# Optimization experiments

Measured on AMD Instinct MI355X. Metric: run time of the kernel, lower is better.

Reference implementation:

```python
import jax, jax.numpy as jnp
import numpy as np

B, S, D = 2, 1024, 1024
L, E, F = 2, 8, 2048


def setup_inputs() -> dict:
    key = jax.random.key(0)
    kx, kp, k1, k2 = jax.random.split(key, 4)
    x = jax.random.normal(kx, (B, S, D), dtype=jnp.float32)
    # prototypes scaled so dot products are O(1), keeping softmax well-behaved
    protos = jax.random.normal(kp, (L, E, D), dtype=jnp.float32) / np.sqrt(D)
    W1 = jax.random.normal(k1, (L, E, D, F), dtype=jnp.float32) * 0.02
    W2 = jax.random.normal(k2, (L, E, F, D), dtype=jnp.float32) * 0.02
    return {"x": x, "protos": protos, "W1": W1, "W2": W2, "k": 2}


def _route(x, protos_l, k):
    # expert_mapping: abs(dot(prototype, input)) per expert, keep top-k, rest -> -inf, softmax
    scores = jnp.abs(jnp.einsum("bsd,ed->bse", x, protos_l))  # [B,S,E]
    topv, _ = jax.lax.top_k(scores, k)
    thresh = topv[..., -1:]  # k-th largest per token
    masked = jnp.where(scores >= thresh, scores, -jnp.inf)
    return jax.nn.softmax(masked, axis=-1)  # [B,S,E]


def reference(x, protos, W1, W2, k):
    n_layers = protos.shape[0]
    for l in range(n_layers):  # fixed small layer loop
        w = _route(x, protos[l], k)  # [B,S,E]
        h = jax.nn.relu(jnp.einsum("bsd,edf->bsef", x, W1[l]))  # [B,S,E,F]
        y = jnp.einsum("bsef,efd,bse->bsd", h, W2[l], w)  # weighted expert mix
        x = x + y
    return x
```

## Files before the change

kernel.cpp:

```cpp
#include <hip/hip_runtime.h>
#include <hip/hip_bf16.h>
#include <cstdint>

#define T_TOKENS 2048
#define DDIM 1024
#define FDIM 2048
#define NEXP 8
#define BMPAD 64
#define RMAX 4608
#define RALLOC 4736

#define ATILE_EL 2048
#define BTILE_EL 4096

typedef unsigned short u16;
typedef short bf16x8 __attribute__((ext_vector_type(8)));
typedef u16 u16x8 __attribute__((ext_vector_type(8)));
typedef u16 u16x4v __attribute__((ext_vector_type(4)));
typedef float f32x4 __attribute__((ext_vector_type(4)));

#define VMCNT(n) asm volatile("s_waitcnt vmcnt(" #n ")" ::: "memory")
#define SB() __builtin_amdgcn_sched_barrier(0)
#define BAR() __builtin_amdgcn_s_barrier()

__device__ __forceinline__ u16 bf16_rn(float f) {
  unsigned u = __builtin_bit_cast(unsigned, f);
  u += 0x7fffu + ((u >> 16) & 1u);
  return (u16)(u >> 16);
}
__device__ __forceinline__ float bf16_f(u16 h) {
  unsigned u = ((unsigned)h) << 16;
  return __builtin_bit_cast(float, u);
}
__device__ __forceinline__ void gl16(const void* g, void* l) {
  __builtin_amdgcn_global_load_lds((const __attribute__((address_space(1))) void*)g,
                                   (__attribute__((address_space(3))) void*)l, 16, 0, 0);
}

template <int GX, int GY, int GZ>
__device__ __forceinline__ void swz3(unsigned lin, int& bx, int& by, int& bz) {
  constexpr unsigned nwg = (unsigned)GX * GY * GZ;
  const unsigned nl = (lin & 7u) * (nwg >> 3) + (lin >> 3);
  bx = nl % GX;
  const unsigned t = nl / GX;
  by = t % GY;
  bz = t / GY;
}


template <bool LO>
__device__ __forceinline__ void wconv_dev(
    int nb, int kb, int e, const float* __restrict__ W, u16* __restrict__ Hi,
    u16* __restrict__ Lo, int K, int N, float* tile ) {
  const float* Wp = W + ((size_t)e * K + (size_t)kb * 32) * N + nb * 128;
  const int t = threadIdx.x;
#pragma unroll
  for (int i = 0; i < 4; ++i) {
    const int f4 = i * 256 + t;
    const int kr = f4 >> 5;
    const int c4 = (f4 & 31) * 4;
    float4 v = *(const float4*)(Wp + (size_t)kr * N + c4);
    *(float4*)&tile[kr * 129 + c4] = v;
  }
  __syncthreads();
  const size_t tb = (((size_t)e * (N >> 7) + nb) * (K >> 5) + kb) * BTILE_EL;
#pragma unroll
  for (int j = 0; j < 2; ++j) {
    const int cid = j * 256 + t;
    const int n = cid & 127, ksel = cid >> 7;
    u16x8 hv, lv;
#pragma unroll
    for (int i = 0; i < 8; ++i) {
      float f = tile[(ksel * 8 + i) * 129 + n];
      u16 h = bf16_rn(f);
      hv[i] = h;
      if (LO) lv[i] = bf16_rn(f - bf16_f(h));
    }
    *(u16x8*)(Hi + tb + (size_t)cid * 8) = hv;
    if (LO) *(u16x8*)(Lo + tb + (size_t)cid * 8) = lv;
  }
}

__device__ __forceinline__ void wconv_p_dev(
    int nb, int kb, int e, const float* __restrict__ W, u16* __restrict__ Hi,
    const float* __restrict__ proto2, float* __restrict__ Ppart, int K, int N,
    float* smem) {
  float* tile = smem;
  float* pr = smem + 32 * 129;
  const float* Wp = W + ((size_t)e * K + (size_t)kb * 32) * N + nb * 128;
  const int t = threadIdx.x;
#pragma unroll
  for (int i = 0; i < 4; ++i) {
    const int f4 = i * 256 + t;
    const int kr = f4 >> 5;
    const int c4 = (f4 & 31) * 4;
    float4 v = *(const float4*)(Wp + (size_t)kr * N + c4);
    *(float4*)&tile[kr * 129 + c4] = v;
  }
  {
    const int idx = t * 4;
    const int e2 = idx >> 7, n = idx & 127;
    *(float4*)&pr[e2 * 128 + n] =
        *(const float4*)(proto2 + (size_t)e2 * DDIM + nb * 128 + n);
  }
  __syncthreads();
  const size_t tb = (((size_t)e * (N >> 7) + nb) * (K >> 5) + kb) * BTILE_EL;
#pragma unroll
  for (int j = 0; j < 2; ++j) {
    const int cid = j * 256 + t;
    const int n = cid & 127, ksel = cid >> 7;
    u16x8 hv;
#pragma unroll
    for (int i = 0; i < 8; ++i) hv[i] = bf16_rn(tile[(ksel * 8 + i) * 129 + n]);
    *(u16x8*)(Hi + tb + (size_t)cid * 8) = hv;
  }
  const int e2 = t >> 5, f = t & 31;
  float s = 0.f;
#pragma unroll 16
  for (int n = 0; n < 128; ++n) s += tile[f * 129 + n] * pr[e2 * 128 + n];
  Ppart[(((size_t)nb * NEXP + e) * NEXP + e2) * FDIM + kb * 32 + f] = s;
}

template <bool LO>
__device__ __forceinline__ void gather_dev(
    int r, const float* __restrict__ x, const int* __restrict__ row2token,
    u16* __restrict__ Ahi, u16* __restrict__ Alo) {
  const int t = row2token[r];
  const int c = threadIdx.x * 4;
  float4 v = make_float4(0.f, 0.f, 0.f, 0.f);
  if (t >= 0) v = *(const float4*)(x + (size_t)t * DDIM + c);
  float vv[4] = {v.x, v.y, v.z, v.w};
  u16x4v hi, lo;
#pragma unroll
  for (int i = 0; i < 4; ++i) {
    u16 h = bf16_rn(vv[i]);
    hi[i] = h;
    if (LO) lo[i] = bf16_rn(vv[i] - bf16_f(h));
  }
  const size_t el = ((size_t)(r >> 6) * (DDIM >> 5) + (c >> 5)) * ATILE_EL +
                    (size_t)(((c >> 3) & 3) * 64 + (r & 63)) * 8 + (c & 7);
  *(u16x4v*)(Ahi + el) = hi;
  if (LO) *(u16x4v*)(Alo + el) = lo;
}

__device__ __forceinline__ void gemm_split_dev(
    unsigned lin, u16* lds, const u16* __restrict__ Ahi, const u16* __restrict__ Alo,
    const u16* __restrict__ Bhi, const u16* __restrict__ Blo,
    u16* __restrict__ OutHi, u16* __restrict__ OutLo,
    const int* __restrict__ cnt, const int* __restrict__ offp, int K, int N) {
  int bx, by, bz;
  swz3<FDIM / 128, RMAX / 64, NEXP>(lin, bx, by, bz);
  const int e = bz;
  const int cp = (cnt[e] + 63) & ~63;
  if (by * 64 >= cp) return;
  const int row0 = offp[e] + by * 64;
  const int n0 = bx * 128;
  const int nkb = K >> 5;
  constexpr int BUF_EL = 12288;

  const int tid = threadIdx.x;
  const int lane = tid & 63;
  const int wid = tid >> 6;
  const int wr = wid >> 1, wc = wid & 1;
  const int lr = lane & 15, kg = lane >> 4;
  const int lo16 = lane << 4;

  f32x4 acc[2][4];
#pragma unroll
  for (int i = 0; i < 2; ++i)
#pragma unroll
    for (int j = 0; j < 4; ++j)
#pragma unroll
      for (int r = 0; r < 4; ++r) acc[i][j][r] = 0.f;

  const size_t abase = (size_t)(row0 >> 6) * nkb;
  const size_t bbase = ((size_t)e * (N >> 7) + (n0 >> 7)) * nkb;

  auto STAGE = [&](int kb, int b) {
    char* d = (char*)(lds + b * BUF_EL);
    const char* gah = (const char*)(Ahi + (abase + kb) * ATILE_EL);
    const char* gal = (const char*)(Alo + (abase + kb) * ATILE_EL);
    const char* gbh = (const char*)(Bhi + (bbase + kb) * BTILE_EL);
    const char* gbl = (const char*)(Blo + (bbase + kb) * BTILE_EL);
    if (wid == 0) {
      gl16(gah + 0 * 1024 + lo16, d + 0 * 1024);
      gl16(gah + 1 * 1024 + lo16, d + 1 * 1024);
      gl16(gah + 2 * 1024 + lo16, d + 2 * 1024);
      gl16(gah + 3 * 1024 + lo16, d + 3 * 1024);
      gl16(gal + 0 * 1024 + lo16, d + 4096 + 0 * 1024);
      gl16(gal + 1 * 1024 + lo16, d + 4096 + 1 * 1024);
    } else if (wid == 1) {
      gl16(gal + 2 * 1024 + lo16, d + 4096 + 2 * 1024);
      gl16(gal + 3 * 1024 + lo16, d + 4096 + 3 * 1024);
      gl16(gbh + 0 * 1024 + lo16, d + 8192 + 0 * 1024);
      gl16(gbh + 1 * 1024 + lo16, d + 8192 + 1 * 1024);
      gl16(gbh + 2 * 1024 + lo16, d + 8192 + 2 * 1024);
      gl16(gbh + 3 * 1024 + lo16, d + 8192 + 3 * 1024);
    } else if (wid == 2) {
      gl16(gbh + 4 * 1024 + lo16, d + 8192 + 4 * 1024);
      gl16(gbh + 5 * 1024 + lo16, d + 8192 + 5 * 1024);
      gl16(gbh + 6 * 1024 + lo16, d + 8192 + 6 * 1024);
      gl16(gbh + 7 * 1024 + lo16, d + 8192 + 7 * 1024);
      gl16(gbl + 0 * 1024 + lo16, d + 16384 + 0 * 1024);
      gl16(gbl + 1 * 1024 + lo16, d + 16384 + 1 * 1024);
    } else {
      gl16(gbl + 2 * 1024 + lo16, d + 16384 + 2 * 1024);
      gl16(gbl + 3 * 1024 + lo16, d + 16384 + 3 * 1024);
      gl16(gbl + 4 * 1024 + lo16, d + 16384 + 4 * 1024);
      gl16(gbl + 5 * 1024 + lo16, d + 16384 + 5 * 1024);
      gl16(gbl + 6 * 1024 + lo16, d + 16384 + 6 * 1024);
      gl16(gbl + 7 * 1024 + lo16, d + 16384 + 7 * 1024);
    }
  };

  STAGE(0, 0);
  int cur = 0;
  for (int kb = 0; kb < nkb; ++kb) {
    const bool pf = (kb + 1 < nkb);
    if (pf) STAGE(kb + 1, cur ^ 1);
    if (pf) { VMCNT(6); } else { VMCNT(0); }
    SB(); BAR(); SB();

    const u16* buf = lds + cur * BUF_EL;
    const u16* AsH = buf;
    const u16* AsL = buf + 2048;
    const u16* BsH = buf + 4096;
    const u16* BsL = buf + 8192;
    const int arow = (kg * 64 + wr * 32 + lr) * 8;
    const int bcol = (kg * 128 + wc * 64 + lr) * 8;

    bf16x8 ah0 = *(const bf16x8*)&AsH[arow];
    bf16x8 ah1 = *(const bf16x8*)&AsH[arow + 128];
    bf16x8 bh[4];
#pragma unroll
    for (int j = 0; j < 4; ++j) bh[j] = *(const bf16x8*)&BsH[bcol + j * 128];
#pragma unroll
    for (int j = 0; j < 4; ++j) {
      acc[0][j] = __builtin_amdgcn_mfma_f32_16x16x32_bf16(ah0, bh[j], acc[0][j], 0, 0, 0);
      acc[1][j] = __builtin_amdgcn_mfma_f32_16x16x32_bf16(ah1, bh[j], acc[1][j], 0, 0, 0);
    }
    bf16x8 al0 = *(const bf16x8*)&AsL[arow];
    bf16x8 al1 = *(const bf16x8*)&AsL[arow + 128];
#pragma unroll
    for (int j = 0; j < 4; ++j) {
      bf16x8 bl = *(const bf16x8*)&BsL[bcol + j * 128];
      acc[0][j] = __builtin_amdgcn_mfma_f32_16x16x32_bf16(ah0, bl, acc[0][j], 0, 0, 0);
      acc[1][j] = __builtin_amdgcn_mfma_f32_16x16x32_bf16(ah1, bl, acc[1][j], 0, 0, 0);
      acc[0][j] = __builtin_amdgcn_mfma_f32_16x16x32_bf16(al0, bh[j], acc[0][j], 0, 0, 0);
      acc[1][j] = __builtin_amdgcn_mfma_f32_16x16x32_bf16(al1, bh[j], acc[1][j], 0, 0, 0);
    }
    SB(); BAR(); SB();
    cur ^= 1;
  }

  const int nkbO = N >> 5;
#pragma unroll
  for (int i = 0; i < 2; ++i) {
#pragma unroll
    for (int j = 0; j < 4; ++j) {
      const int Cj = n0 + wc * 64 + j * 16 + lr;
      f32x4 v = acc[i][j];
#pragma unroll
      for (int r = 0; r < 4; ++r) {
        const int R = row0 + wr * 32 + i * 16 + kg * 4 + r;
        float f = fmaxf(v[r], 0.f);
        const size_t el = ((size_t)(R >> 6) * nkbO + (Cj >> 5)) * ATILE_EL +
                          (size_t)(((Cj >> 3) & 3) * 64 + (R & 63)) * 8 + (Cj & 7);
        u16 h = bf16_rn(f);
        OutHi[el] = h;
        OutLo[el] = bf16_rn(f - bf16_f(h));
      }
    }
  }
}

template <int GX, int GY, bool RELU, int OUTMODE>
__device__ __forceinline__ void gemm_plain_dev(
    unsigned lin, u16* lds, const u16* __restrict__ Ahi, const u16* __restrict__ Bhi,
    u16* __restrict__ OutHi, float* __restrict__ OutF,
    const int* __restrict__ cnt, const int* __restrict__ offp, int K, int N) {
  int bx, by, bz;
  swz3<GX, GY, NEXP>(lin, bx, by, bz);
  const int e = bz;
  const int cp = (cnt[e] + 63) & ~63;
  if (by * 128 >= cp) return;
  const int row0 = offp[e] + by * 128;
  const int rend = offp[e] + cp;
  const int n0 = bx * 128;
  const int nkb = K >> 5;
  constexpr int BUF_EL = 8192;

  const int tid = threadIdx.x;
  const int lane = tid & 63;
  const int wid = tid >> 6;
  const int wr = wid >> 1, wc = wid & 1;
  const int lr = lane & 15, kg = lane >> 4;
  const int lo16 = lane << 4;

  f32x4 acc[4][4];
#pragma unroll
  for (int i = 0; i < 4; ++i)
#pragma unroll
    for (int j = 0; j < 4; ++j)
#pragma unroll
      for (int r = 0; r < 4; ++r) acc[i][j][r] = 0.f;

  const int at0 = row0 >> 6;
  const size_t bbase = ((size_t)e * (N >> 7) + (n0 >> 7)) * nkb;

  auto STAGE = [&](int kb, int b) {
    char* d = (char*)(lds + b * BUF_EL);
    if (wid < 2) {
      const char* g = (const char*)(Ahi + ((size_t)(at0 + wid) * nkb + kb) * ATILE_EL);
      gl16(g + 0 * 1024 + lo16, d + wid * 4096 + 0 * 1024);
      gl16(g + 1 * 1024 + lo16, d + wid * 4096 + 1 * 1024);
      gl16(g + 2 * 1024 + lo16, d + wid * 4096 + 2 * 1024);
      gl16(g + 3 * 1024 + lo16, d + wid * 4096 + 3 * 1024);
    } else {
      const char* g = (const char*)(Bhi + (bbase + kb) * BTILE_EL) + (wid - 2) * 4096;
      gl16(g + 0 * 1024 + lo16, d + 8192 + (wid - 2) * 4096 + 0 * 1024);
      gl16(g + 1 * 1024 + lo16, d + 8192 + (wid - 2) * 4096 + 1 * 1024);
      gl16(g + 2 * 1024 + lo16, d + 8192 + (wid - 2) * 4096 + 2 * 1024);
      gl16(g + 3 * 1024 + lo16, d + 8192 + (wid - 2) * 4096 + 3 * 1024);
    }
  };

  STAGE(0, 0);
  int cur = 0;
  for (int kb = 0; kb < nkb; ++kb) {
    const bool pf = (kb + 1 < nkb);
    if (pf) STAGE(kb + 1, cur ^ 1);
    if (pf) { VMCNT(4); } else { VMCNT(0); }
    SB(); BAR(); SB();

    const u16* buf = lds + cur * BUF_EL;
    const u16* AsH = buf + wr * 2048;
    const u16* BsH = buf + 4096;
    const int arow = (kg * 64 + lr) * 8;
    const int bcol = (kg * 128 + wc * 64 + lr) * 8;

    bf16x8 ah[4], bh[4];
#pragma unroll
    for (int i = 0; i < 4; ++i) ah[i] = *(const bf16x8*)&AsH[arow + i * 128];
#pragma unroll
    for (int j = 0; j < 4; ++j) bh[j] = *(const bf16x8*)&BsH[bcol + j * 128];
#pragma unroll
    for (int i = 0; i < 4; ++i)
#pragma unroll
      for (int j = 0; j < 4; ++j)
        acc[i][j] = __builtin_amdgcn_mfma_f32_16x16x32_bf16(ah[i], bh[j], acc[i][j], 0, 0, 0);
    SB(); BAR(); SB();
    cur ^= 1;
  }

  const int nkbO = N >> 5;
#pragma unroll
  for (int i = 0; i < 4; ++i) {
#pragma unroll
    for (int j = 0; j < 4; ++j) {
      const int Cj = n0 + wc * 64 + j * 16 + lr;
      f32x4 v = acc[i][j];
#pragma unroll
      for (int r = 0; r < 4; ++r) {
        const int R = row0 + wr * 64 + i * 16 + kg * 4 + r;
        if (R >= rend) continue;
        float f = v[r];
        if (RELU) f = fmaxf(f, 0.f);
        if constexpr (OUTMODE == 0) {
          OutF[(size_t)R * N + Cj] = f;
        } else {
          const size_t el = ((size_t)(R >> 6) * nkbO + (Cj >> 5)) * ATILE_EL +
                            (size_t)(((Cj >> 3) & 3) * 64 + (R & 63)) * 8 + (Cj & 7);
          OutHi[el] = bf16_rn(f);
        }
      }
    }
  }
}


__global__ __launch_bounds__(256) void route_kernel(
    const float* __restrict__ x, const float* __restrict__ protos,
    int* __restrict__ eid, float* __restrict__ wgt) {
  const int t = blockIdx.x;
  const int tid = threadIdx.x;
  __shared__ float red[NEXP][256];
  const float4 xv = ((const float4*)(x + (size_t)t * DDIM))[tid];
  float acc[NEXP];
#pragma unroll
  for (int e = 0; e < NEXP; ++e) {
    const float4 p = ((const float4*)protos)[e * 256 + tid];
    acc[e] = xv.x * p.x + xv.y * p.y + xv.z * p.z + xv.w * p.w;
  }
#pragma unroll
  for (int e = 0; e < NEXP; ++e) red[e][tid] = acc[e];
  __syncthreads();
  for (int s = 128; s > 0; s >>= 1) {
    if (tid < s) {
#pragma unroll
      for (int e = 0; e < NEXP; ++e) red[e][tid] += red[e][tid + s];
    }
    __syncthreads();
  }
  if (tid == 0) {
    float m1 = -1.f, m2 = -1.f;
    int i1 = 0, i2 = 0;
#pragma unroll
    for (int e = 0; e < NEXP; ++e) {
      float s = fabsf(red[e][0]);
      if (s > m1) { m2 = m1; i2 = i1; m1 = s; i1 = e; }
      else if (s > m2) { m2 = s; i2 = e; }
    }
    float e2 = __expf(m2 - m1);
    float z = 1.f + e2;
    eid[t * 2] = i1;
    eid[t * 2 + 1] = i2;
    wgt[t * 2] = 1.f / z;
    wgt[t * 2 + 1] = e2 / z;
  }
}

__global__ __launch_bounds__(256) void route2_kernel(
    const float* __restrict__ x, const float* __restrict__ protos2,
    const u16* __restrict__ h_hi, const u16* __restrict__ h_lo,
    const float* __restrict__ P, const int* __restrict__ eidA,
    const int* __restrict__ pos, const float* __restrict__ wgtA,
    int* __restrict__ eidB, float* __restrict__ wgtB) {
  const int t = blockIdx.x;
  const int tid = threadIdx.x;
  __shared__ float red[NEXP][256];
  const float4 xv = ((const float4*)(x + (size_t)t * DDIM))[tid];
  float acc[NEXP];
#pragma unroll
  for (int e = 0; e < NEXP; ++e) {
    const float4 p = ((const float4*)protos2)[e * 256 + tid];
    acc[e] = xv.x * p.x + xv.y * p.y + xv.z * p.z + xv.w * p.w;
  }
  const int p0 = pos[t * 2], p1 = pos[t * 2 + 1];
  const int e0 = eidA[t * 2], e1 = eidA[t * 2 + 1];
  const float w0 = wgtA[t * 2], w1 = wgtA[t * 2 + 1];
  const int f0 = tid * 8;
  const int nkbF = FDIM >> 5;
  float h0[8], h1[8];
  {
    const size_t el0 = ((size_t)(p0 >> 6) * nkbF + (f0 >> 5)) * ATILE_EL +
                       (size_t)((((f0 >> 3) & 3) * 64 + (p0 & 63)) * 8);
    const size_t el1 = ((size_t)(p1 >> 6) * nkbF + (f0 >> 5)) * ATILE_EL +
                       (size_t)((((f0 >> 3) & 3) * 64 + (p1 & 63)) * 8);
    u16x8 a = *(const u16x8*)&h_hi[el0], b = *(const u16x8*)&h_lo[el0];
    u16x8 c = *(const u16x8*)&h_hi[el1], d = *(const u16x8*)&h_lo[el1];
#pragma unroll
    for (int j = 0; j < 8; ++j) {
      h0[j] = bf16_f(a[j]) + bf16_f(b[j]);
      h1[j] = bf16_f(c[j]) + bf16_f(d[j]);
    }
  }
#pragma unroll
  for (int e2 = 0; e2 < NEXP; ++e2) {
    const float* P0 = P + ((size_t)(e0 * NEXP + e2)) * FDIM + f0;
    const float* P1 = P + ((size_t)(e1 * NEXP + e2)) * FDIM + f0;
    float c = 0.f;
#pragma unroll
    for (int j = 0; j < 8; ++j) c += w0 * h0[j] * P0[j] + w1 * h1[j] * P1[j];
    acc[e2] += c;
  }
#pragma unroll
  for (int e = 0; e < NEXP; ++e) red[e][tid] = acc[e];
  __syncthreads();
  for (int s = 128; s > 0; s >>= 1) {
    if (tid < s) {
#pragma unroll
      for (int e = 0; e < NEXP; ++e) red[e][tid] += red[e][tid + s];
    }
    __syncthreads();
  }
  if (tid == 0) {
    float m1 = -1.f, m2 = -1.f;
    int i1 = 0, i2 = 0;
#pragma unroll
    for (int e = 0; e < NEXP; ++e) {
      float s = fabsf(red[e][0]);
      if (s > m1) { m2 = m1; i2 = i1; m1 = s; i1 = e; }
      else if (s > m2) { m2 = s; i2 = e; }
    }
    float e2 = __expf(m2 - m1);
    float z = 1.f + e2;
    eidB[t * 2] = i1;
    eidB[t * 2 + 1] = i2;
    wgtB[t * 2] = 1.f / z;
    wgtB[t * 2 + 1] = e2 / z;
  }
}

__device__ __forceinline__ void compact_dev(
    const int* __restrict__ eid, int* __restrict__ cnt, int* __restrict__ offp,
    int* __restrict__ row2token, int* __restrict__ pos, int* lcnt ) {
  int* s_off = lcnt + NEXP * 256;
  int* s_tot = s_off + NEXP;
  const int tid = threadIdx.x;
  const int base = tid * 16;
  int my[16];
#pragma unroll
  for (int i = 0; i < 4; ++i)
    *(int4*)&my[i * 4] = *(const int4*)(eid + base + i * 4);
#pragma unroll
  for (int e = 0; e < NEXP; ++e) {
    int c = 0;
#pragma unroll
    for (int i = 0; i < 16; ++i) c += (my[i] == e) ? 1 : 0;
    lcnt[e * 256 + tid] = c;
  }
  for (int r = tid; r < RMAX; r += 256) row2token[r] = -1;
  __syncthreads();
  if (tid < NEXP) {
    int run = 0;
    for (int i = 0; i < 256; ++i) {
      int v = lcnt[tid * 256 + i];
      lcnt[tid * 256 + i] = run;
      run += v;
    }
    s_tot[tid] = run;
  }
  __syncthreads();
  if (tid == 0) {
    int o = 0;
    for (int e = 0; e < NEXP; ++e) {
      s_off[e] = o;
      o += (s_tot[e] + BMPAD - 1) & ~(BMPAD - 1);
    }
  }
  __syncthreads();
  int myoff[NEXP];
#pragma unroll
  for (int e = 0; e < NEXP; ++e) myoff[e] = s_off[e] + lcnt[e * 256 + tid];
#pragma unroll
  for (int i = 0; i < 16; ++i) {
    int r = 0;
#pragma unroll
    for (int e = 0; e < NEXP; ++e) r = (my[i] == e) ? myoff[e] : r;
    row2token[r] = (base + i) >> 1;
    pos[base + i] = r;
#pragma unroll
    for (int e = 0; e < NEXP; ++e) myoff[e] += (my[i] == e) ? 1 : 0;
  }
  if (tid < NEXP) {
    cnt[tid] = s_tot[tid];
    offp[tid] = s_off[tid];
  }
}

__global__ __launch_bounds__(256) void compact_kernel(
    const int* __restrict__ eid, int* __restrict__ cnt, int* __restrict__ offp,
    int* __restrict__ row2token, int* __restrict__ pos) {
  __shared__ int lcnt[NEXP * 256 + 16];
  compact_dev(eid, cnt, offp, row2token, pos, lcnt);
}

__global__ __launch_bounds__(256) void fusedC1_kernel(
    const float* __restrict__ W1, u16* __restrict__ W_hi, u16* __restrict__ W_lo,
    const float* __restrict__ x, const int* __restrict__ row2token,
    u16* __restrict__ Ag_hi, u16* __restrict__ Ag_lo) {
  __shared__ float smem[32 * 129];
  const unsigned lin = blockIdx.x;
  if (lin < 4096u) {
    const int nb = lin % 16;
    const int kb = (lin / 16) % 32;
    const int e = lin / 512;
    wconv_dev<true>(nb, kb, e, W1, W_hi, W_lo, DDIM, FDIM, smem);
  } else {
    gather_dev<true>((int)(lin - 4096u), x, row2token, Ag_hi, Ag_lo);
  }
}

__global__ __launch_bounds__(256, 3) void fusedC2_kernel(
    const u16* __restrict__ Ag_hi, const u16* __restrict__ Ag_lo,
    const u16* __restrict__ W_hi, const u16* __restrict__ W_lo,
    u16* __restrict__ h_hi, u16* __restrict__ h_lo,
    const int* __restrict__ cnt, const int* __restrict__ offp,
    const float* __restrict__ W2, u16* __restrict__ W2A,
    const float* __restrict__ proto2, float* __restrict__ Ppart) {
  __shared__ u16 lds[2 * 12288];
  const unsigned lin = blockIdx.x;
  if (lin < 9216u) {
    gemm_split_dev(lin, lds, Ag_hi, Ag_lo, W_hi, W_lo, h_hi, h_lo, cnt, offp,
                   DDIM, FDIM);
  } else {
    const unsigned l2 = lin - 9216u;
    const int nb = l2 % 8;
    const int kb = (l2 / 8) % 64;
    const int e = l2 / 512;
    wconv_p_dev(nb, kb, e, W2, W2A, proto2, Ppart, FDIM, DDIM, (float*)lds);
  }
}

__global__ __launch_bounds__(256, 4) void fusedC3_kernel(
    const u16* __restrict__ h_hi, const u16* __restrict__ W2A,
    float* __restrict__ part, const int* __restrict__ cnt, const int* __restrict__ offp,
    const float* __restrict__ W1b, u16* __restrict__ W_lo,
    const float* __restrict__ W2b, u16* __restrict__ W_hi,
    const float* __restrict__ Ppart, float* __restrict__ P) {
  __shared__ u16 lds[2 * 8192];
  const unsigned lin = blockIdx.x;
  if (lin < 2304u) {
    gemm_plain_dev<DDIM / 128, RMAX / 128, false, 0>(
        lin, lds, h_hi, W2A, nullptr, part, cnt, offp, FDIM, DDIM);
  } else if (lin < 6400u) {
    const unsigned l2 = lin - 2304u;
    wconv_dev<false>(l2 % 16, (l2 / 16) % 32, l2 / 512, W1b, W_lo, nullptr,
                     DDIM, FDIM, (float*)lds);
  } else if (lin < 10496u) {
    const unsigned l2 = lin - 6400u;
    wconv_dev<false>(l2 % 8, (l2 / 8) % 64, l2 / 512, W2b, W_hi, nullptr,
                     FDIM, DDIM, (float*)lds);
  } else {
    const int i = (int)(lin - 10496u) * 256 + threadIdx.x;
    float s = 0.f;
#pragma unroll
    for (int nb = 0; nb < 8; ++nb) s += Ppart[(size_t)nb * (NEXP * NEXP * FDIM) + i];
    P[i] = s;
  }
}

__global__ __launch_bounds__(256) void fusedD_kernel(
    const float* __restrict__ part, const int* __restrict__ pos,
    const float* __restrict__ wgt, float* __restrict__ x,
    const int* __restrict__ eidB, int* __restrict__ cnt, int* __restrict__ offp,
    int* __restrict__ row2token, int* __restrict__ posB) {
  __shared__ int lcnt[NEXP * 256 + 16];
  const unsigned lin = blockIdx.x;
  if (lin < 2048u) {
    const int t = lin;
    const int c = threadIdx.x * 4;
    const int p0 = pos[t * 2], p1 = pos[t * 2 + 1];
    const float w0 = wgt[t * 2], w1 = wgt[t * 2 + 1];
    float4 xa = *(float4*)(x + (size_t)t * DDIM + c);
    const float4 y0 = *(const float4*)(part + (size_t)p0 * DDIM + c);
    const float4 y1 = *(const float4*)(part + (size_t)p1 * DDIM + c);
    xa.x += w0 * y0.x + w1 * y1.x;
    xa.y += w0 * y0.y + w1 * y1.y;
    xa.z += w0 * y0.z + w1 * y1.z;
    xa.w += w0 * y0.w + w1 * y1.w;
    *(float4*)(x + (size_t)t * DDIM + c) = xa;
  } else {
    compact_dev(eidB, cnt, offp, row2token, posB, lcnt);
  }
}

__global__ __launch_bounds__(256) void gather_kernel(
    const float* __restrict__ x, const int* __restrict__ row2token,
    u16* __restrict__ Ahi) {
  gather_dev<false>(blockIdx.x, x, row2token, Ahi, nullptr);
}

template <int GX, bool RELU, int OUTMODE>
__global__ __launch_bounds__(256, 4) void gemm_plain_kernel(
    const u16* __restrict__ Ahi, const u16* __restrict__ Bhi,
    u16* __restrict__ OutHi, float* __restrict__ OutF,
    const int* __restrict__ cnt, const int* __restrict__ offp, int K, int N) {
  __shared__ u16 lds[2 * 8192];
  gemm_plain_dev<GX, RMAX / 128, RELU, OUTMODE>(blockIdx.x, lds, Ahi, Bhi, OutHi,
                                                OutF, cnt, offp, K, N);
}

__global__ __launch_bounds__(256) void apply_kernel(
    const float* __restrict__ part, const int* __restrict__ pos,
    const float* __restrict__ wgt, float* __restrict__ x) {
  const int t = blockIdx.x;
  const int c = threadIdx.x * 4;
  const int p0 = pos[t * 2], p1 = pos[t * 2 + 1];
  const float w0 = wgt[t * 2], w1 = wgt[t * 2 + 1];
  float4 xa = *(float4*)(x + (size_t)t * DDIM + c);
  const float4 y0 = *(const float4*)(part + (size_t)p0 * DDIM + c);
  const float4 y1 = *(const float4*)(part + (size_t)p1 * DDIM + c);
  xa.x += w0 * y0.x + w1 * y1.x;
  xa.y += w0 * y0.y + w1 * y1.y;
  xa.z += w0 * y0.z + w1 * y1.z;
  xa.w += w0 * y0.w + w1 * y1.w;
  *(float4*)(x + (size_t)t * DDIM + c) = xa;
}

extern "C" void kernel_launch(void* const* d_in, const int* in_sizes, int n_in,
                              void* d_out, int out_size, void* d_ws, size_t ws_size,
                              hipStream_t stream) {
  const float* x = (const float*)d_in[0];
  const float* protos = (const float*)d_in[1];
  const float* W1 = (const float*)d_in[2];
  const float* W2 = (const float*)d_in[3];
  float* xcur = (float*)d_out;

  u16* W_hi = (u16*)d_ws;
  u16* W_lo = W_hi + (size_t)NEXP * DDIM * FDIM;
  u16* W2A = W_lo + (size_t)NEXP * DDIM * FDIM;
  u16* Ag_hi = W2A + (size_t)NEXP * DDIM * FDIM;
  u16* Ag_lo = Ag_hi + (size_t)RALLOC * DDIM;
  u16* h_hi = Ag_lo + (size_t)RALLOC * DDIM;
  u16* h_lo = h_hi + (size_t)RALLOC * FDIM;
  float* part = (float*)(h_lo + (size_t)RALLOC * FDIM);
  float* Ppart = part + (size_t)RALLOC * DDIM;
  float* P = Ppart + (size_t)8 * NEXP * NEXP * FDIM;
  float* wgtA = P + (size_t)NEXP * NEXP * FDIM;
  float* wgtB = wgtA + T_TOKENS * 2;
  int* eidA = (int*)(wgtB + T_TOKENS * 2);
  int* eidB = eidA + T_TOKENS * 2;
  int* posA = eidB + T_TOKENS * 2;
  int* posB = posA + T_TOKENS * 2;
  int* cnt = posB + T_TOKENS * 2;
  int* offp = cnt + NEXP;
  int* row2token = offp + NEXP;

  hipMemcpyAsync(xcur, x, (size_t)T_TOKENS * DDIM * sizeof(float),
                 hipMemcpyDeviceToDevice, stream);

  const float* protos2 = protos + (size_t)NEXP * DDIM;
  const float* W1b = W1 + (size_t)NEXP * DDIM * FDIM;
  const float* W2b = W2 + (size_t)NEXP * FDIM * DDIM;

  route_kernel<<<T_TOKENS, 256, 0, stream>>>(xcur, protos, eidA, wgtA);
  compact_kernel<<<1, 256, 0, stream>>>(eidA, cnt, offp, row2token, posA);
  fusedC1_kernel<<<4096 + RMAX, 256, 0, stream>>>(
      W1, W_hi, W_lo, xcur, row2token, Ag_hi, Ag_lo);
  fusedC2_kernel<<<9216 + 4096, 256, 0, stream>>>(
      Ag_hi, Ag_lo, W_hi, W_lo, h_hi, h_lo, cnt, offp, W2, W2A, protos2, Ppart);
  fusedC3_kernel<<<2304 + 4096 + 4096 + 512, 256, 0, stream>>>(
      h_hi, W2A, part, cnt, offp, W1b, W_lo, W2b, W_hi, Ppart, P);
  route2_kernel<<<T_TOKENS, 256, 0, stream>>>(
      xcur, protos2, h_hi, h_lo, P, eidA, posA, wgtA, eidB, wgtB);
  fusedD_kernel<<<2048 + 1, 256, 0, stream>>>(
      part, posA, wgtA, xcur, eidB, cnt, offp, row2token, posB);

  gather_kernel<<<RMAX, 256, 0, stream>>>(xcur, row2token, Ag_hi);
  gemm_plain_kernel<FDIM / 128, true, 2><<<(FDIM / 128) * (RMAX / 128) * NEXP, 256, 0, stream>>>(
      Ag_hi, W_lo, h_hi, nullptr, cnt, offp, DDIM, FDIM);
  gemm_plain_kernel<DDIM / 128, false, 0><<<(DDIM / 128) * (RMAX / 128) * NEXP, 256, 0, stream>>>(
      h_hi, W_hi, nullptr, part, cnt, offp, FDIM, DDIM);
  apply_kernel<<<T_TOKENS, 256, 0, stream>>>(part, posB, wgtB, xcur);
}
```

Measured before the change: 331.3 us.

## Reschedule weight conversions into routing kernel and drop input copy

Moves layer-1 routing, the W2 conversion (with the prototype projection partials) and the W1 conversion into one fused first kernel, so the weight prep overlaps routing instead of sharing launches with the gathers and GEMMs. The gather and P reduction now form their own kernel, and C2/C3 become pure GEMM or GEMM-plus-layer-2 conversions. It also removes the device-to-device copy of x by reading the input directly and writing the residual into the output buffer in fusedD. The trade-off is that the first kernel grows large, and the GEMM stages lose the conversion work that used to fill idle CUs.

```diff
diff --git a/kernel.cpp b/kernel.cpp
--- a/kernel.cpp
+++ b/kernel.cpp
@@ -48,10 +48,49 @@
 }
 
 
+__device__ __forceinline__ void route_dev(
+    int t, const float* __restrict__ x, const float* __restrict__ protos,
+    int* __restrict__ eid, float* __restrict__ wgt, float* red) {
+  const int tid = threadIdx.x;
+  const float4 xv = ((const float4*)(x + (size_t)t * DDIM))[tid];
+  float acc[NEXP];
+#pragma unroll
+  for (int e = 0; e < NEXP; ++e) {
+    const float4 p = ((const float4*)protos)[e * 256 + tid];
+    acc[e] = xv.x * p.x + xv.y * p.y + xv.z * p.z + xv.w * p.w;
+  }
+#pragma unroll
+  for (int e = 0; e < NEXP; ++e) red[e * 256 + tid] = acc[e];
+  __syncthreads();
+  for (int s = 128; s > 0; s >>= 1) {
+    if (tid < s) {
+#pragma unroll
+      for (int e = 0; e < NEXP; ++e) red[e * 256 + tid] += red[e * 256 + tid + s];
+    }
+    __syncthreads();
+  }
+  if (tid == 0) {
+    float m1 = -1.f, m2 = -1.f;
+    int i1 = 0, i2 = 0;
+#pragma unroll
+    for (int e = 0; e < NEXP; ++e) {
+      float s = fabsf(red[e * 256]);
+      if (s > m1) { m2 = m1; i2 = i1; m1 = s; i1 = e; }
+      else if (s > m2) { m2 = s; i2 = e; }
+    }
+    float e2 = __expf(m2 - m1);
+    float z = 1.f + e2;
+    eid[t * 2] = i1;
+    eid[t * 2 + 1] = i2;
+    wgt[t * 2] = 1.f / z;
+    wgt[t * 2 + 1] = e2 / z;
+  }
+}
+
 template <bool LO>
 __device__ __forceinline__ void wconv_dev(
     int nb, int kb, int e, const float* __restrict__ W, u16* __restrict__ Hi,
-    u16* __restrict__ Lo, int K, int N, float* tile ) {
+    u16* __restrict__ Lo, int K, int N, float* tile) {
   const float* Wp = W + ((size_t)e * K + (size_t)kb * 32) * N + nb * 128;
   const int t = threadIdx.x;
 #pragma unroll
@@ -378,45 +417,136 @@
   }
 }
 
-
-__global__ __launch_bounds__(256) void route_kernel(
-    const float* __restrict__ x, const float* __restrict__ protos,
-    int* __restrict__ eid, float* __restrict__ wgt) {
-  const int t = blockIdx.x;
+__device__ __forceinline__ void compact_dev(
+    const int* __restrict__ eid, int* __restrict__ cnt, int* __restrict__ offp,
+    int* __restrict__ row2token, int* __restrict__ pos, int* lcnt) {
+  int* s_off = lcnt + NEXP * 256;
+  int* s_tot = s_off + NEXP;
   const int tid = threadIdx.x;
-  __shared__ float red[NEXP][256];
-  const float4 xv = ((const float4*)(x + (size_t)t * DDIM))[tid];
-  float acc[NEXP];
+  const int base = tid * 16;
+  int my[16];
+#pragma unroll
+  for (int i = 0; i < 4; ++i)
+    *(int4*)&my[i * 4] = *(const int4*)(eid + base + i * 4);
 #pragma unroll
   for (int e = 0; e < NEXP; ++e) {
-    const float4 p = ((const float4*)protos)[e * 256 + tid];
-    acc[e] = xv.x * p.x + xv.y * p.y + xv.z * p.z + xv.w * p.w;
-  }
-#pragma unroll
-  for (int e = 0; e < NEXP; ++e) red[e][tid] = acc[e];
+    int c = 0;
+#pragma unroll
+    for (int i = 0; i < 16; ++i) c += (my[i] == e) ? 1 : 0;
+    lcnt[e * 256 + tid] = c;
+  }
+  for (int r = tid; r < RMAX; r += 256) row2token[r] = -1;
   __syncthreads();
-  for (int s = 128; s > 0; s >>= 1) {
-    if (tid < s) {
-#pragma unroll
-      for (int e = 0; e < NEXP; ++e) red[e][tid] += red[e][tid + s];
-    }
-    __syncthreads();
-  }
+  if (tid < NEXP) {
+    int run = 0;
+    for (int i = 0; i < 256; ++i) {
+      int v = lcnt[tid * 256 + i];
+      lcnt[tid * 256 + i] = run;
+      run += v;
+    }
+    s_tot[tid] = run;
+  }
+  __syncthreads();
   if (tid == 0) {
-    float m1 = -1.f, m2 = -1.f;
-    int i1 = 0, i2 = 0;
-#pragma unroll
+    int o = 0;
     for (int e = 0; e < NEXP; ++e) {
-      float s = fabsf(red[e][0]);
-      if (s > m1) { m2 = m1; i2 = i1; m1 = s; i1 = e; }
-      else if (s > m2) { m2 = s; i2 = e; }
-    }
-    float e2 = __expf(m2 - m1);
-    float z = 1.f + e2;
-    eid[t * 2] = i1;
-    eid[t * 2 + 1] = i2;
-    wgt[t * 2] = 1.f / z;
-    wgt[t * 2 + 1] = e2 / z;
+      s_off[e] = o;
+      o += (s_tot[e] + BMPAD - 1) & ~(BMPAD - 1);
+    }
+  }
+  __syncthreads();
+  int myoff[NEXP];
+#pragma unroll
+  for (int e = 0; e < NEXP; ++e) myoff[e] = s_off[e] + lcnt[e * 256 + tid];
+#pragma unroll
+  for (int i = 0; i < 16; ++i) {
+    int r = 0;
+#pragma unroll
+    for (int e = 0; e < NEXP; ++e) r = (my[i] == e) ? myoff[e] : r;
+    row2token[r] = (base + i) >> 1;
+    pos[base + i] = r;
+#pragma unroll
+    for (int e = 0; e < NEXP; ++e) myoff[e] += (my[i] == e) ? 1 : 0;
+  }
+  if (tid < NEXP) {
+    cnt[tid] = s_tot[tid];
+    offp[tid] = s_off[tid];
+  }
+}
+
+
+__global__ __launch_bounds__(256) void fusedK1_kernel(
+    const float* __restrict__ xin, const float* __restrict__ protos,
+    int* __restrict__ eidA, float* __restrict__ wgtA,
+    const float* __restrict__ W2, u16* __restrict__ W2A,
+    const float* __restrict__ proto2, float* __restrict__ Ppart,
+    const float* __restrict__ W1, u16* __restrict__ W_hi, u16* __restrict__ W_lo) {
+  __shared__ float smem[32 * 129 + 8 * 128];
+  const unsigned lin = blockIdx.x;
+  if (lin < 2048u) {
+    route_dev((int)lin, xin, protos, eidA, wgtA, smem);
+  } else if (lin < 6144u) {
+    const unsigned l2 = lin - 2048u;
+    wconv_p_dev(l2 % 8, (l2 / 8) % 64, l2 / 512, W2, W2A, proto2, Ppart,
+                FDIM, DDIM, smem);
+  } else {
+    const unsigned l3 = lin - 6144u;
+    wconv_dev<true>(l3 % 16, (l3 / 16) % 32, l3 / 512, W1, W_hi, W_lo,
+                    DDIM, FDIM, smem);
+  }
+}
+
+__global__ __launch_bounds__(256) void compact_kernel(
+    const int* __restrict__ eid, int* __restrict__ cnt, int* __restrict__ offp,
+    int* __restrict__ row2token, int* __restrict__ pos) {
+  __shared__ int lcnt[NEXP * 256 + 16];
+  compact_dev(eid, cnt, offp, row2token, pos, lcnt);
+}
+
+__global__ __launch_bounds__(256) void fusedK3_kernel(
+    const float* __restrict__ xin, const int* __restrict__ row2token,
+    u16* __restrict__ Ag_hi, u16* __restrict__ Ag_lo,
+    const float* __restrict__ Ppart, float* __restrict__ P) {
+  const unsigned lin = blockIdx.x;
+  if (lin < (unsigned)RMAX) {
+    gather_dev<true>((int)lin, xin, row2token, Ag_hi, Ag_lo);
+  } else {
+    const int i = (int)(lin - RMAX) * 256 + threadIdx.x;
+    float s = 0.f;
+#pragma unroll
+    for (int nb = 0; nb < 8; ++nb) s += Ppart[(size_t)nb * (NEXP * NEXP * FDIM) + i];
+    P[i] = s;
+  }
+}
+
+__global__ __launch_bounds__(256, 3) void fusedC2_kernel(
+    const u16* __restrict__ Ag_hi, const u16* __restrict__ Ag_lo,
+    const u16* __restrict__ W_hi, const u16* __restrict__ W_lo,
+    u16* __restrict__ h_hi, u16* __restrict__ h_lo,
+    const int* __restrict__ cnt, const int* __restrict__ offp) {
+  __shared__ u16 lds[2 * 12288];
+  gemm_split_dev(blockIdx.x, lds, Ag_hi, Ag_lo, W_hi, W_lo, h_hi, h_lo, cnt, offp,
+                 DDIM, FDIM);
+}
+
+__global__ __launch_bounds__(256, 4) void fusedC3_kernel(
+    const u16* __restrict__ h_hi, const u16* __restrict__ W2A,
+    float* __restrict__ part, const int* __restrict__ cnt, const int* __restrict__ offp,
+    const float* __restrict__ W1b, u16* __restrict__ W_lo,
+    const float* __restrict__ W2b, u16* __restrict__ W_hi) {
+  __shared__ u16 lds[2 * 8192];
+  const unsigned lin = blockIdx.x;
+  if (lin < 2304u) {
+    gemm_plain_dev<DDIM / 128, RMAX / 128, false, 0>(
+        lin, lds, h_hi, W2A, nullptr, part, cnt, offp, FDIM, DDIM);
+  } else if (lin < 6400u) {
+    const unsigned l2 = lin - 2304u;
+    wconv_dev<false>(l2 % 16, (l2 / 16) % 32, l2 / 512, W1b, W_lo, nullptr,
+                     DDIM, FDIM, (float*)lds);
+  } else {
+    const unsigned l2 = lin - 6400u;
+    wconv_dev<false>(l2 % 8, (l2 / 8) % 64, l2 / 512, W2b, W_hi, nullptr,
+                     FDIM, DDIM, (float*)lds);
   }
 }
 
@@ -492,138 +622,10 @@
   }
 }
 
-__device__ __forceinline__ void compact_dev(
-    const int* __restrict__ eid, int* __restrict__ cnt, int* __restrict__ offp,
-    int* __restrict__ row2token, int* __restrict__ pos, int* lcnt ) {
-  int* s_off = lcnt + NEXP * 256;
-  int* s_tot = s_off + NEXP;
-  const int tid = threadIdx.x;
-  const int base = tid * 16;
-  int my[16];
-#pragma unroll
-  for (int i = 0; i < 4; ++i)
-    *(int4*)&my[i * 4] = *(const int4*)(eid + base + i * 4);
-#pragma unroll
-  for (int e = 0; e < NEXP; ++e) {
-    int c = 0;
-#pragma unroll
-    for (int i = 0; i < 16; ++i) c += (my[i] == e) ? 1 : 0;
-    lcnt[e * 256 + tid] = c;
-  }
-  for (int r = tid; r < RMAX; r += 256) row2token[r] = -1;
-  __syncthreads();
-  if (tid < NEXP) {
-    int run = 0;
-    for (int i = 0; i < 256; ++i) {
-      int v = lcnt[tid * 256 + i];
-      lcnt[tid * 256 + i] = run;
-      run += v;
-    }
-    s_tot[tid] = run;
-  }
-  __syncthreads();
-  if (tid == 0) {
-    int o = 0;
-    for (int e = 0; e < NEXP; ++e) {
-      s_off[e] = o;
-      o += (s_tot[e] + BMPAD - 1) & ~(BMPAD - 1);
-    }
-  }
-  __syncthreads();
-  int myoff[NEXP];
-#pragma unroll
-  for (int e = 0; e < NEXP; ++e) myoff[e] = s_off[e] + lcnt[e * 256 + tid];
-#pragma unroll
-  for (int i = 0; i < 16; ++i) {
-    int r = 0;
-#pragma unroll
-    for (int e = 0; e < NEXP; ++e) r = (my[i] == e) ? myoff[e] : r;
-    row2token[r] = (base + i) >> 1;
-    pos[base + i] = r;
-#pragma unroll
-    for (int e = 0; e < NEXP; ++e) myoff[e] += (my[i] == e) ? 1 : 0;
-  }
-  if (tid < NEXP) {
-    cnt[tid] = s_tot[tid];
-    offp[tid] = s_off[tid];
-  }
-}
-
-__global__ __launch_bounds__(256) void compact_kernel(
-    const int* __restrict__ eid, int* __restrict__ cnt, int* __restrict__ offp,
-    int* __restrict__ row2token, int* __restrict__ pos) {
-  __shared__ int lcnt[NEXP * 256 + 16];
-  compact_dev(eid, cnt, offp, row2token, pos, lcnt);
-}
-
-__global__ __launch_bounds__(256) void fusedC1_kernel(
-    const float* __restrict__ W1, u16* __restrict__ W_hi, u16* __restrict__ W_lo,
-    const float* __restrict__ x, const int* __restrict__ row2token,
-    u16* __restrict__ Ag_hi, u16* __restrict__ Ag_lo) {
-  __shared__ float smem[32 * 129];
-  const unsigned lin = blockIdx.x;
-  if (lin < 4096u) {
-    const int nb = lin % 16;
-    const int kb = (lin / 16) % 32;
-    const int e = lin / 512;
-    wconv_dev<true>(nb, kb, e, W1, W_hi, W_lo, DDIM, FDIM, smem);
-  } else {
-    gather_dev<true>((int)(lin - 4096u), x, row2token, Ag_hi, Ag_lo);
-  }
-}
-
-__global__ __launch_bounds__(256, 3) void fusedC2_kernel(
-    const u16* __restrict__ Ag_hi, const u16* __restrict__ Ag_lo,
-    const u16* __restrict__ W_hi, const u16* __restrict__ W_lo,
-    u16* __restrict__ h_hi, u16* __restrict__ h_lo,
-    const int* __restrict__ cnt, const int* __restrict__ offp,
-    const float* __restrict__ W2, u16* __restrict__ W2A,
-    const float* __restrict__ proto2, float* __restrict__ Ppart) {
-  __shared__ u16 lds[2 * 12288];
-  const unsigned lin = blockIdx.x;
-  if (lin < 9216u) {
-    gemm_split_dev(lin, lds, Ag_hi, Ag_lo, W_hi, W_lo, h_hi, h_lo, cnt, offp,
-                   DDIM, FDIM);
-  } else {
-    const unsigned l2 = lin - 9216u;
-    const int nb = l2 % 8;
-    const int kb = (l2 / 8) % 64;
-    const int e = l2 / 512;
-    wconv_p_dev(nb, kb, e, W2, W2A, proto2, Ppart, FDIM, DDIM, (float*)lds);
-  }
-}
-
-__global__ __launch_bounds__(256, 4) void fusedC3_kernel(
-    const u16* __restrict__ h_hi, const u16* __restrict__ W2A,
-    float* __restrict__ part, const int* __restrict__ cnt, const int* __restrict__ offp,
-    const float* __restrict__ W1b, u16* __restrict__ W_lo,
-    const float* __restrict__ W2b, u16* __restrict__ W_hi,
-    const float* __restrict__ Ppart, float* __restrict__ P) {
-  __shared__ u16 lds[2 * 8192];
-  const unsigned lin = blockIdx.x;
-  if (lin < 2304u) {
-    gemm_plain_dev<DDIM / 128, RMAX / 128, false, 0>(
-        lin, lds, h_hi, W2A, nullptr, part, cnt, offp, FDIM, DDIM);
-  } else if (lin < 6400u) {
-    const unsigned l2 = lin - 2304u;
-    wconv_dev<false>(l2 % 16, (l2 / 16) % 32, l2 / 512, W1b, W_lo, nullptr,
-                     DDIM, FDIM, (float*)lds);
-  } else if (lin < 10496u) {
-    const unsigned l2 = lin - 6400u;
-    wconv_dev<false>(l2 % 8, (l2 / 8) % 64, l2 / 512, W2b, W_hi, nullptr,
-                     FDIM, DDIM, (float*)lds);
-  } else {
-    const int i = (int)(lin - 10496u) * 256 + threadIdx.x;
-    float s = 0.f;
-#pragma unroll
-    for (int nb = 0; nb < 8; ++nb) s += Ppart[(size_t)nb * (NEXP * NEXP * FDIM) + i];
-    P[i] = s;
-  }
-}
-
 __global__ __launch_bounds__(256) void fusedD_kernel(
     const float* __restrict__ part, const int* __restrict__ pos,
-    const float* __restrict__ wgt, float* __restrict__ x,
+    const float* __restrict__ wgt, const float* __restrict__ xin,
+    float* __restrict__ xcur,
     const int* __restrict__ eidB, int* __restrict__ cnt, int* __restrict__ offp,
     int* __restrict__ row2token, int* __restrict__ posB) {
   __shared__ int lcnt[NEXP * 256 + 16];
@@ -633,14 +635,14 @@
     const int c = threadIdx.x * 4;
     const int p0 = pos[t * 2], p1 = pos[t * 2 + 1];
     const float w0 = wgt[t * 2], w1 = wgt[t * 2 + 1];
-    float4 xa = *(float4*)(x + (size_t)t * DDIM + c);
+    float4 xa = *(const float4*)(xin + (size_t)t * DDIM + c);
     const float4 y0 = *(const float4*)(part + (size_t)p0 * DDIM + c);
     const float4 y1 = *(const float4*)(part + (size_t)p1 * DDIM + c);
     xa.x += w0 * y0.x + w1 * y1.x;
     xa.y += w0 * y0.y + w1 * y1.y;
     xa.z += w0 * y0.z + w1 * y1.z;
     xa.w += w0 * y0.w + w1 * y1.w;
-    *(float4*)(x + (size_t)t * DDIM + c) = xa;
+    *(float4*)(xcur + (size_t)t * DDIM + c) = xa;
   } else {
     compact_dev(eidB, cnt, offp, row2token, posB, lcnt);
   }
@@ -682,7 +684,7 @@
 extern "C" void kernel_launch(void* const* d_in, const int* in_sizes, int n_in,
                               void* d_out, int out_size, void* d_ws, size_t ws_size,
                               hipStream_t stream) {
-  const float* x = (const float*)d_in[0];
+  const float* xin = (const float*)d_in[0];
   const float* protos = (const float*)d_in[1];
   const float* W1 = (const float*)d_in[2];
   const float* W2 = (const float*)d_in[3];
@@ -708,30 +710,30 @@
   int* offp = cnt + NEXP;
   int* row2token = offp + NEXP;
 
-  hipMemcpyAsync(xcur, x, (size_t)T_TOKENS * DDIM * sizeof(float),
-                 hipMemcpyDeviceToDevice, stream);
-
   const float* protos2 = protos + (size_t)NEXP * DDIM;
   const float* W1b = W1 + (size_t)NEXP * DDIM * FDIM;
   const float* W2b = W2 + (size_t)NEXP * FDIM * DDIM;
 
-  route_kernel<<<T_TOKENS, 256, 0, stream>>>(xcur, protos, eidA, wgtA);
+  fusedK1_kernel<<<2048 + 4096 + 4096, 256, 0, stream>>>(
+      xin, protos, eidA, wgtA, W2, W2A, protos2, Ppart, W1, W_hi, W_lo);
   compact_kernel<<<1, 256, 0, stream>>>(eidA, cnt, offp, row2token, posA);
-  fusedC1_kernel<<<4096 + RMAX, 256, 0, stream>>>(
-      W1, W_hi, W_lo, xcur, row2token, Ag_hi, Ag_lo);
-  fusedC2_kernel<<<9216 + 4096, 256, 0, stream>>>(
-      Ag_hi, Ag_lo, W_hi, W_lo, h_hi, h_lo, cnt, offp, W2, W2A, protos2, Ppart);
-  fusedC3_kernel<<<2304 + 4096 + 4096 + 512, 256, 0, stream>>>(
-      h_hi, W2A, part, cnt, offp, W1b, W_lo, W2b, W_hi, Ppart, P);
+  fusedK3_kernel<<<RMAX + 512, 256, 0, stream>>>(
+      xin, row2token, Ag_hi, Ag_lo, Ppart, P);
+  fusedC2_kernel<<<(FDIM / 128) * (RMAX / 64) * NEXP, 256, 0, stream>>>(
+      Ag_hi, Ag_lo, W_hi, W_lo, h_hi, h_lo, cnt, offp);
+  fusedC3_kernel<<<2304 + 4096 + 4096, 256, 0, stream>>>(
+      h_hi, W2A, part, cnt, offp, W1b, W_lo, W2b, W_hi);
   route2_kernel<<<T_TOKENS, 256, 0, stream>>>(
-      xcur, protos2, h_hi, h_lo, P, eidA, posA, wgtA, eidB, wgtB);
+      xin, protos2, h_hi, h_lo, P, eidA, posA, wgtA, eidB, wgtB);
   fusedD_kernel<<<2048 + 1, 256, 0, stream>>>(
-      part, posA, wgtA, xcur, eidB, cnt, offp, row2token, posB);
+      part, posA, wgtA, xin, xcur, eidB, cnt, offp, row2token, posB);
 
   gather_kernel<<<RMAX, 256, 0, stream>>>(xcur, row2token, Ag_hi);
-  gemm_plain_kernel<FDIM / 128, true, 2><<<(FDIM / 128) * (RMAX / 128) * NEXP, 256, 0, stream>>>(
-      Ag_hi, W_lo, h_hi, nullptr, cnt, offp, DDIM, FDIM);
-  gemm_plain_kernel<DDIM / 128, false, 0><<<(DDIM / 128) * (RMAX / 128) * NEXP, 256, 0, stream>>>(
-      h_hi, W_hi, nullptr, part, cnt, offp, FDIM, DDIM);
+  gemm_plain_kernel<FDIM / 128, true, 2>
+      <<<(FDIM / 128) * (RMAX / 128) * NEXP, 256, 0, stream>>>(
+          Ag_hi, W_lo, h_hi, nullptr, cnt, offp, DDIM, FDIM);
+  gemm_plain_kernel<DDIM / 128, false, 0>
+      <<<(DDIM / 128) * (RMAX / 128) * NEXP, 256, 0, stream>>>(
+          h_hi, W_hi, nullptr, part, cnt, offp, FDIM, DDIM);
   apply_kernel<<<T_TOKENS, 256, 0, stream>>>(part, posB, wgtB, xcur);
 }
```

Result: no change. 331.3 us (-0.0%).
